# Optimization experiments

Measured on AMD Instinct MI355X. Metric: run time of the kernel, lower is better.

The kernel has to match this reference:

```python
import jax, jax.numpy as jnp
import numpy as np

EPS = 1e-6


def _mlp(x, W1, b1, W2, b2):
    # x: [b,s]; W1: [m,s,h]; W2: [m,h,o] -> [m,b,o]  (m = stacked module dim)
    h = jnp.tanh(jnp.einsum('bs,msh->mbh', x, W1) + b1[:, None, :])
    return jnp.einsum('mbh,mho->mbo', h, W2) + b2[:, None, :]


def _ln(x, g, b):
    mu = jnp.mean(x, axis=-1, keepdims=True)
    var = jnp.var(x, axis=-1, keepdims=True)
    return g * (x - mu) / jnp.sqrt(var + EPS) + b


def setup_inputs() -> dict:
    B, S, H, E, R, L = 1024, 256, 512, 64, 32, 9
    key = jax.random.key(0)
    ks = jax.random.split(key, 8)

    def xavier(k, shape):
        bound = np.sqrt(6.0 / (shape[-2] + shape[-1])).astype(np.float32)
        return jax.random.uniform(k, shape, jnp.float32, -bound, bound)

    return {
        'query_embed': jax.random.normal(ks[0], (B, S), jnp.float32),
        'tpr': jax.random.normal(ks[1], (B, E, R, E), jnp.float32) * 0.1,
        'eW1': xavier(ks[2], (2, S, H)), 'eb1': jnp.zeros((2, H), jnp.float32),
        'eW2': xavier(ks[3], (2, H, E)), 'eb2': jnp.zeros((2, E), jnp.float32),
        'rW1': xavier(ks[4], (3, S, H)), 'rb1': jnp.zeros((3, H), jnp.float32),
        'rW2': xavier(ks[5], (3, H, R)), 'rb2': jnp.zeros((3, R), jnp.float32),
        'ln_g': jnp.ones((3, E), jnp.float32), 'ln_b': jnp.zeros((3, E), jnp.float32),
        'Z': xavier(ks[6], (E, L)),
    }


def reference(query_embed, tpr, eW1, eb1, eW2, eb2, rW1, rb1, rW2, rb2, ln_g, ln_b, Z):
    e = _mlp(query_embed, eW1, eb1, eW2, eb2)   # [2,B,E] (e[1] unused, as in original)
    r = _mlp(query_embed, rW1, rb1, rW2, rb2)   # [3,B,R]
    i1 = _ln(jnp.einsum('be,br,berf->bf', e[0], r[0], tpr), ln_g[0], ln_b[0])
    i2 = _ln(jnp.einsum('be,br,berf->bf', i1, r[1], tpr), ln_g[1], ln_b[1])
    i3 = _ln(jnp.einsum('be,br,berf->bf', i2, r[2], tpr), ln_g[2], ln_b[2])
    step_sum = i1 + i2 + i3
    return jnp.einsum('bf,fl->bl', step_sum, Z)
```

## Files before the change

### kernel.cpp

```cpp
#include <hip/hip_runtime.h>
#include <math.h>

#define B_  1024
#define S_  256
#define H_  512
#define E_  64
#define R_  32
#define L_  9
#define EPS_ 1e-6f
#define TB  8

__global__ __launch_bounds__(256) void mlp_kernel(
    const float* __restrict__ x,
    const float* __restrict__ eW1, const float* __restrict__ eb1,
    const float* __restrict__ eW2, const float* __restrict__ eb2,
    const float* __restrict__ rW1, const float* __restrict__ rb1,
    const float* __restrict__ rW2, const float* __restrict__ rb2,
    float* __restrict__ e0_out,
    float* __restrict__ r_out)
{
    __shared__ __align__(16) float xs[TB][S_];
    __shared__ __align__(16) float hs[TB][H_];
    const int t  = threadIdx.x;
    const int b0 = blockIdx.x * TB;
    const int m  = blockIdx.y;

    {
        const float4* x4 = (const float4*)(x + (size_t)b0 * S_);
        float4* xs4 = (float4*)&xs[0][0];
        xs4[t]       = x4[t];
        xs4[t + 256] = x4[t + 256];
    }
    __syncthreads();

    const float* W1 = (m == 0) ? eW1 : (rW1 + (size_t)(m - 1) * S_ * H_);
    const float* b1 = (m == 0) ? eb1 : (rb1 + (size_t)(m - 1) * H_);

    float acc0[TB], acc1[TB];
    #pragma unroll
    for (int bb = 0; bb < TB; ++bb) { acc0[bb] = 0.0f; acc1[bb] = 0.0f; }

    for (int s4 = 0; s4 < S_ / 4; ++s4) {
        const float* Wp = W1 + (size_t)(4 * s4) * H_ + t;
        float wa0 = Wp[0];          float wb0 = Wp[256];
        float wa1 = Wp[H_];         float wb1 = Wp[H_ + 256];
        float wa2 = Wp[2 * H_];     float wb2 = Wp[2 * H_ + 256];
        float wa3 = Wp[3 * H_];     float wb3 = Wp[3 * H_ + 256];
        #pragma unroll
        for (int bb = 0; bb < TB; ++bb) {
            float4 xv = ((const float4*)&xs[bb][0])[s4];
            acc0[bb] = fmaf(xv.x, wa0, acc0[bb]);
            acc1[bb] = fmaf(xv.x, wb0, acc1[bb]);
            acc0[bb] = fmaf(xv.y, wa1, acc0[bb]);
            acc1[bb] = fmaf(xv.y, wb1, acc1[bb]);
            acc0[bb] = fmaf(xv.z, wa2, acc0[bb]);
            acc1[bb] = fmaf(xv.z, wb2, acc1[bb]);
            acc0[bb] = fmaf(xv.w, wa3, acc0[bb]);
            acc1[bb] = fmaf(xv.w, wb3, acc1[bb]);
        }
    }
    float bias0 = b1[t], bias1 = b1[t + 256];
    #pragma unroll
    for (int bb = 0; bb < TB; ++bb) {
        hs[bb][t]       = tanhf(acc0[bb] + bias0);
        hs[bb][t + 256] = tanhf(acc1[bb] + bias1);
    }
    __syncthreads();

    if (m == 0) {
        const float* W2 = eW2;
        const float* b2 = eb2;
        int o  = t & 63;
        int bq = t >> 6;
        #pragma unroll
        for (int i = 0; i < TB / 4; ++i) {
            int bb = bq + i * 4;
            float a0 = 0.f, a1 = 0.f, a2 = 0.f, a3 = 0.f;
            #pragma unroll 4
            for (int j = 0; j < H_; j += 4) {
                float4 hv = ((const float4*)&hs[bb][0])[j >> 2];
                a0 = fmaf(hv.x, W2[(size_t)(j + 0) * E_ + o], a0);
                a1 = fmaf(hv.y, W2[(size_t)(j + 1) * E_ + o], a1);
                a2 = fmaf(hv.z, W2[(size_t)(j + 2) * E_ + o], a2);
                a3 = fmaf(hv.w, W2[(size_t)(j + 3) * E_ + o], a3);
            }
            e0_out[(size_t)(b0 + bb) * E_ + o] = b2[o] + ((a0 + a1) + (a2 + a3));
        }
    } else {
        const float* W2 = rW2 + (size_t)(m - 1) * H_ * R_;
        const float* b2 = rb2 + (size_t)(m - 1) * R_;
        int o  = t & 31;
        int bb = t >> 5;
        float a0 = 0.f, a1 = 0.f, a2 = 0.f, a3 = 0.f;
        #pragma unroll 4
        for (int j = 0; j < H_; j += 4) {
            float4 hv = ((const float4*)&hs[bb][0])[j >> 2];
            a0 = fmaf(hv.x, W2[(size_t)(j + 0) * R_ + o], a0);
            a1 = fmaf(hv.y, W2[(size_t)(j + 1) * R_ + o], a1);
            a2 = fmaf(hv.z, W2[(size_t)(j + 2) * R_ + o], a2);
            a3 = fmaf(hv.w, W2[(size_t)(j + 3) * R_ + o], a3);
        }
        r_out[((size_t)(m - 1) * B_ + (b0 + bb)) * R_ + o] = b2[o] + ((a0 + a1) + (a2 + a3));
    }
}

__global__ __launch_bounds__(256) void tpr_kernel(
    const float* __restrict__ tpr,
    const float* __restrict__ e0,
    const float* __restrict__ rws,
    const float* __restrict__ ln_g,
    const float* __restrict__ ln_b,
    const float* __restrict__ Z,
    float* __restrict__ out)
{
    __shared__ __align__(16) float M[2][E_][E_];
    __shared__ __align__(16) float red[16][E_];
    __shared__ float xcur[E_];
    __shared__ float ssum_sh[E_];
    __shared__ float rsh[3][R_];
    __shared__ float e0sh[E_];

    const int t = threadIdx.x;
    const int b = blockIdx.x;

    if (t < 96) { int k = t >> 5, j = t & 31; rsh[k][j] = rws[((size_t)k * B_ + b) * R_ + j]; }
    if (t < E_) e0sh[t] = e0[(size_t)b * E_ + t];
    __syncthreads();

    const float4* tpr4 = (const float4*)(tpr + (size_t)b * E_ * R_ * E_);
    const int f4 = t & 15;
    const int eg = t >> 4;

    float4 a0[4], a1[4], a2[4];
    #pragma unroll
    for (int ep = 0; ep < 4; ++ep) {
        a0[ep] = (float4){0, 0, 0, 0};
        a1[ep] = (float4){0, 0, 0, 0};
        a2[ep] = (float4){0, 0, 0, 0};
    }

    #pragma unroll 4
    for (int r = 0; r < R_; ++r) {
        float w0 = rsh[0][r], w1 = rsh[1][r], w2 = rsh[2][r];
        #pragma unroll
        for (int ep = 0; ep < 4; ++ep) {
            float4 v = tpr4[(eg + 16 * ep) * 512 + r * 16 + f4];
            a0[ep].x = fmaf(w0, v.x, a0[ep].x); a0[ep].y = fmaf(w0, v.y, a0[ep].y);
            a0[ep].z = fmaf(w0, v.z, a0[ep].z); a0[ep].w = fmaf(w0, v.w, a0[ep].w);
            a1[ep].x = fmaf(w1, v.x, a1[ep].x); a1[ep].y = fmaf(w1, v.y, a1[ep].y);
            a1[ep].z = fmaf(w1, v.z, a1[ep].z); a1[ep].w = fmaf(w1, v.w, a1[ep].w);
            a2[ep].x = fmaf(w2, v.x, a2[ep].x); a2[ep].y = fmaf(w2, v.y, a2[ep].y);
            a2[ep].z = fmaf(w2, v.z, a2[ep].z); a2[ep].w = fmaf(w2, v.w, a2[ep].w);
        }
    }

    float4 t0p = {0, 0, 0, 0};
    #pragma unroll
    for (int ep = 0; ep < 4; ++ep) {
        int e = eg + 16 * ep;
        ((float4*)&M[0][e][0])[f4] = a1[ep];
        ((float4*)&M[1][e][0])[f4] = a2[ep];
        float ev = e0sh[e];
        t0p.x = fmaf(ev, a0[ep].x, t0p.x); t0p.y = fmaf(ev, a0[ep].y, t0p.y);
        t0p.z = fmaf(ev, a0[ep].z, t0p.z); t0p.w = fmaf(ev, a0[ep].w, t0p.w);
    }
    ((float4*)&red[eg][0])[f4] = t0p;
    __syncthreads();

    if (t < E_) {
        const int f = t;
        float acc = 0.0f;
        #pragma unroll
        for (int g = 0; g < 16; ++g) acc += red[g][f];

        float ssum = 0.0f;
        #pragma unroll
        for (int k = 0; k < 3; ++k) {
            float s = acc;
            #pragma unroll
            for (int off = 32; off >= 1; off >>= 1) s += __shfl_xor(s, off, 64);
            float mu = s * (1.0f / 64.0f);
            float d = acc - mu;
            float vs = d * d;
            #pragma unroll
            for (int off = 32; off >= 1; off >>= 1) vs += __shfl_xor(vs, off, 64);
            float var = vs * (1.0f / 64.0f);
            float iv = ln_g[k * E_ + f] * d * rsqrtf(var + EPS_) + ln_b[k * E_ + f];
            ssum += iv;
            if (k < 2) {
                xcur[f] = iv;
                float n0 = 0.f, n1 = 0.f, n2 = 0.f, n3 = 0.f;
                #pragma unroll 4
                for (int e = 0; e < E_; e += 4) {
                    n0 = fmaf(xcur[e + 0], M[k][e + 0][f], n0);
                    n1 = fmaf(xcur[e + 1], M[k][e + 1][f], n1);
                    n2 = fmaf(xcur[e + 2], M[k][e + 2][f], n2);
                    n3 = fmaf(xcur[e + 3], M[k][e + 3][f], n3);
                }
                acc = (n0 + n1) + (n2 + n3);
            }
        }
        ssum_sh[f] = ssum;

        if (t < L_) {
            float o = 0.0f;
            #pragma unroll
            for (int f2 = 0; f2 < E_; ++f2)
                o = fmaf(ssum_sh[f2], Z[f2 * L_ + t], o);
            out[(size_t)b * L_ + t] = o;
        }
    }
}

extern "C" void kernel_launch(void* const* d_in, const int* in_sizes, int n_in,
                              void* d_out, int out_size, void* d_ws, size_t ws_size,
                              hipStream_t stream) {
    const float* x    = (const float*)d_in[0];
    const float* tpr  = (const float*)d_in[1];
    const float* eW1  = (const float*)d_in[2];
    const float* eb1  = (const float*)d_in[3];
    const float* eW2  = (const float*)d_in[4];
    const float* eb2  = (const float*)d_in[5];
    const float* rW1  = (const float*)d_in[6];
    const float* rb1  = (const float*)d_in[7];
    const float* rW2  = (const float*)d_in[8];
    const float* rb2  = (const float*)d_in[9];
    const float* ln_g = (const float*)d_in[10];
    const float* ln_b = (const float*)d_in[11];
    const float* Z    = (const float*)d_in[12];
    float* out = (float*)d_out;

    float* e0_ws = (float*)d_ws;
    float* r_ws  = e0_ws + (size_t)B_ * E_;

    dim3 g1(B_ / TB, 4);
    mlp_kernel<<<g1, 256, 0, stream>>>(x, eW1, eb1, eW2, eb2,
                                       rW1, rb1, rW2, rb2, e0_ws, r_ws);
    tpr_kernel<<<B_, 256, 0, stream>>>(tpr, e0_ws, r_ws, ln_g, ln_b, Z, out);
}
```

Measured before the change: 779.0 us.

## Remap tpr reduction so each wave reads contiguous 1KB rows and shuffles over r

Changes the tpr_kernel thread-to-data mapping so each wave handles 16 e-rows and reads fully contiguous 1KB chunks (4 r values × 16 float4) per load, instead of 16-float4 strided segments. Partial sums over r are combined with cross-lane xor shuffles, and the e0 reduction buffer shrinks from 16 to 4 rows. The goal is more coalesced, streaming access to the 512MB tpr tensor, which dominates the runtime, at the cost of extra shuffle instructions and an inner el loop.

Result: faster. 748.1 us (-4.0%).

```diff
diff --git a/kernel.cpp b/kernel.cpp
--- a/kernel.cpp
+++ b/kernel.cpp
@@ -114,7 +114,7 @@
     float* __restrict__ out)
 {
     __shared__ __align__(16) float M[2][E_][E_];
-    __shared__ __align__(16) float red[16][E_];
+    __shared__ __align__(16) float red[4][E_];
     __shared__ float xcur[E_];
     __shared__ float ssum_sh[E_];
     __shared__ float rsh[3][R_];
@@ -127,51 +127,58 @@
     if (t < E_) e0sh[t] = e0[(size_t)b * E_ + t];
     __syncthreads();
 
-    const float4* tpr4 = (const float4*)(tpr + (size_t)b * E_ * R_ * E_);
-    const int f4 = t & 15;
-    const int eg = t >> 4;
-
-    float4 a0[4], a1[4], a2[4];
+    const int w  = t >> 6;
+    const int j  = t & 63;
+    const int jh = j >> 4;
+    const float4* base = (const float4*)(tpr + (size_t)b * E_ * R_ * E_) + w * 8192;
+
+    float wk0[8], wk1[8], wk2[8];
     #pragma unroll
-    for (int ep = 0; ep < 4; ++ep) {
-        a0[ep] = (float4){0, 0, 0, 0};
-        a1[ep] = (float4){0, 0, 0, 0};
-        a2[ep] = (float4){0, 0, 0, 0};
-    }
-
-    #pragma unroll 4
-    for (int r = 0; r < R_; ++r) {
-        float w0 = rsh[0][r], w1 = rsh[1][r], w2 = rsh[2][r];
-        #pragma unroll
-        for (int ep = 0; ep < 4; ++ep) {
-            float4 v = tpr4[(eg + 16 * ep) * 512 + r * 16 + f4];
-            a0[ep].x = fmaf(w0, v.x, a0[ep].x); a0[ep].y = fmaf(w0, v.y, a0[ep].y);
-            a0[ep].z = fmaf(w0, v.z, a0[ep].z); a0[ep].w = fmaf(w0, v.w, a0[ep].w);
-            a1[ep].x = fmaf(w1, v.x, a1[ep].x); a1[ep].y = fmaf(w1, v.y, a1[ep].y);
-            a1[ep].z = fmaf(w1, v.z, a1[ep].z); a1[ep].w = fmaf(w1, v.w, a1[ep].w);
-            a2[ep].x = fmaf(w2, v.x, a2[ep].x); a2[ep].y = fmaf(w2, v.y, a2[ep].y);
-            a2[ep].z = fmaf(w2, v.z, a2[ep].z); a2[ep].w = fmaf(w2, v.w, a2[ep].w);
-        }
+    for (int it = 0; it < 8; ++it) {
+        int r = it * 4 + jh;
+        wk0[it] = rsh[0][r]; wk1[it] = rsh[1][r]; wk2[it] = rsh[2][r];
     }
 
     float4 t0p = {0, 0, 0, 0};
-    #pragma unroll
-    for (int ep = 0; ep < 4; ++ep) {
-        int e = eg + 16 * ep;
-        ((float4*)&M[0][e][0])[f4] = a1[ep];
-        ((float4*)&M[1][e][0])[f4] = a2[ep];
+    for (int el = 0; el < 16; ++el) {
+        float4 a0 = {0,0,0,0}, a1 = {0,0,0,0}, a2 = {0,0,0,0};
+        #pragma unroll
+        for (int it = 0; it < 8; ++it) {
+            float4 v = base[el * 512 + it * 64 + j];
+            float w0 = wk0[it], w1 = wk1[it], w2 = wk2[it];
+            a0.x = fmaf(w0, v.x, a0.x); a0.y = fmaf(w0, v.y, a0.y);
+            a0.z = fmaf(w0, v.z, a0.z); a0.w = fmaf(w0, v.w, a0.w);
+            a1.x = fmaf(w1, v.x, a1.x); a1.y = fmaf(w1, v.y, a1.y);
+            a1.z = fmaf(w1, v.z, a1.z); a1.w = fmaf(w1, v.w, a1.w);
+            a2.x = fmaf(w2, v.x, a2.x); a2.y = fmaf(w2, v.y, a2.y);
+            a2.z = fmaf(w2, v.z, a2.z); a2.w = fmaf(w2, v.w, a2.w);
+        }
+        #pragma unroll
+        for (int st = 16; st <= 32; st <<= 1) {
+            a0.x += __shfl_xor(a0.x, st); a0.y += __shfl_xor(a0.y, st);
+            a0.z += __shfl_xor(a0.z, st); a0.w += __shfl_xor(a0.w, st);
+            a1.x += __shfl_xor(a1.x, st); a1.y += __shfl_xor(a1.y, st);
+            a1.z += __shfl_xor(a1.z, st); a1.w += __shfl_xor(a1.w, st);
+            a2.x += __shfl_xor(a2.x, st); a2.y += __shfl_xor(a2.y, st);
+            a2.z += __shfl_xor(a2.z, st); a2.w += __shfl_xor(a2.w, st);
+        }
+        const int e = w * 16 + el;
+        if (j < 16) {
+            ((float4*)&M[0][e][0])[j] = a1;
+            ((float4*)&M[1][e][0])[j] = a2;
+        }
         float ev = e0sh[e];
-        t0p.x = fmaf(ev, a0[ep].x, t0p.x); t0p.y = fmaf(ev, a0[ep].y, t0p.y);
-        t0p.z = fmaf(ev, a0[ep].z, t0p.z); t0p.w = fmaf(ev, a0[ep].w, t0p.w);
-    }
-    ((float4*)&red[eg][0])[f4] = t0p;
+        t0p.x = fmaf(ev, a0.x, t0p.x); t0p.y = fmaf(ev, a0.y, t0p.y);
+        t0p.z = fmaf(ev, a0.z, t0p.z); t0p.w = fmaf(ev, a0.w, t0p.w);
+    }
+    if (j < 16) ((float4*)&red[w][0])[j] = t0p;
     __syncthreads();
 
     if (t < E_) {
         const int f = t;
         float acc = 0.0f;
         #pragma unroll
-        for (int g = 0; g < 16; ++g) acc += red[g][f];
+        for (int g = 0; g < 4; ++g) acc += red[g][f];
 
         float ssum = 0.0f;
         #pragma unroll
```
